# Performance work log

Measured on AMD Instinct MI355X. Metric: run time of the kernel, lower is better.

The kernel has to match this reference:

```python
import jax, jax.numpy as jnp
from jax import lax
import numpy as np

GAMMA = 0.01
ALPHA = 1.0
Z_MU = 0.0
Z_NORM = 1.0
NUM_ITER = 100
TOL = 1e-6
GUESS_RATIO = 1.0 - 0.001


def kernel_inv(Z_norm2, ZU_norm2, gamma, alpha):
    # Z_norm2, ZU_norm2: (N,1). Secant root solve per point, with the
    # original host-side early break emulated by a per-scan 'done' flag so the
    # math matches the torch loop exactly (carry freezes once converged).
    ZUperp_norm2 = Z_norm2 - ZU_norm2
    exp_gammaz = jnp.exp(-gamma * ZU_norm2)

    def f(x):
        return (1.0 - alpha * exp_gammaz * jnp.exp(-gamma * x)) ** 2 * x - ZUperp_norm2

    def body(carry, _):
        x_m2, x_m1, done = carry
        f_m1 = f(x_m1)
        f_m2 = f(x_m2)
        f_diff = f_m1 - f_m2
        small = jnp.abs(f_diff) < TOL
        f_diff = jnp.where(small, jnp.where(f_diff >= 0, TOL, -TOL), f_diff)
        x = x_m1 - f_m1 * (x_m1 - x_m2) / f_diff
        step_size = jnp.max(jnp.abs(x - x_m1))
        new_m2 = jnp.where(done, x_m2, x_m1)
        new_m1 = jnp.where(done, x_m1, x)
        done = done | (step_size < TOL)
        return (new_m2, new_m1, done), None

    init = (ZUperp_norm2 * GUESS_RATIO, ZUperp_norm2, jnp.array(False))
    (_, x, _), _ = lax.scan(body, init, None, length=NUM_ITER)
    return alpha * jnp.exp(-gamma * (ZU_norm2 + x))


def setup_inputs() -> dict:
    key = jax.random.key(0)
    kz, ku, kv, km, kc = jax.random.split(key, 5)
    N, D, K = 100000, 512, 32
    Z_all = jax.random.normal(kz, (N, D), dtype=jnp.float32)
    U, _ = jnp.linalg.qr(jax.random.normal(ku, (D, K), dtype=jnp.float32))  # orthonormal basis (D,k)
    V = jax.random.normal(kv, (D, K * (K + 1) // 2), dtype=jnp.float32) * 0.01
    z_mu_local = jax.random.normal(km, (D,), dtype=jnp.float32)
    x_c = jax.random.normal(kc, (D,), dtype=jnp.float32)
    choice_index = jnp.arange(N, dtype=jnp.int32)
    return {"Z_all": Z_all, "U": U, "V": V, "z_mu_local": z_mu_local,
            "x_c": x_c, "choice_index": choice_index}


def reference(Z_all, U, V, z_mu_local, x_c, choice_index):
    D, k = U.shape
    Z_all = Z_all * Z_NORm if False else Z_all * Z_NORM + Z_MU
    Z = Z_all[choice_index]                       # (N,D)
    ZU = Z @ U                                    # (N,k)
    x_muU = z_mu_local @ U                        # (k,)
    x_cU = x_c @ U                                # (k,)
    change = x_c - z_mu_local - (x_cU - x_muU) @ U.T  # (D,)
    Z_norm2 = jnp.sum((Z - z_mu_local) ** 2, axis=1, keepdims=True)   # (N,1)
    ZU_norm2 = jnp.sum((ZU - x_muU) ** 2, axis=1, keepdims=True)      # (N,1)
    kernel = kernel_inv(Z_norm2, ZU_norm2, GAMMA, ALPHA)              # (N,1)
    coord = ZU - x_cU                                                 # (N,k)
    iu0, iu1 = np.triu_indices(k)
    H_input = coord[:, iu0] * coord[:, iu1]       # (N, k(k+1)/2) -- upper-tri of outer products
    Xhat = Z + kernel * (change + H_input @ V.T)  # (N,D)
    return Z_all.at[choice_index].set(Xhat)
```

## Files before the change

kernel.cpp:

```cpp
#include <hip/hip_runtime.h>
#include <stdint.h>

#define NROW 100000
#define DDIM 512
#define NPAIR 528
#define PK 544
#define BR 32
#define NBLK 3125
#define GAMMA 0.01f
#define ALPHA 1.0f
#define TOLR 1e-6f
#define GUESS 0.999f

using f32x4  = __attribute__((ext_vector_type(4))) float;
using s16x8  = __attribute__((ext_vector_type(8))) short;
using us16x4 = __attribute__((ext_vector_type(4))) unsigned short;
typedef unsigned short ushort_t;
typedef unsigned int   uint_t;

#define WS_XMUU   0
#define WS_XCU    128
#define WS_MUN    256
#define WS_CHANGE 512
#define WS_UB     4096
#define WS_VB     53248
#define WS_IU     610304

#define ZB_STR   520
#define HB_STR   552
#define SM_ZU    35328
#define SM_CIDX  39680
#define SM_XMU   39808
#define SM_XCU   39936
#define SM_TOTAL 40064

__device__ __forceinline__ ushort_t f2bf(float x) {
    uint_t u = __builtin_bit_cast(uint_t, x);
    u += 0x7fffu + ((u >> 16) & 1u);
    return (ushort_t)(u >> 16);
}

__global__ __launch_bounds__(256) void kernelA(const float* __restrict__ U,
                                               const float* __restrict__ V,
                                               const float* __restrict__ zmu,
                                               const float* __restrict__ xc,
                                               char* __restrict__ ws) {
    int t = threadIdx.x;
    if (blockIdx.x == 0) {
        __shared__ float redMu[8][32], redC[8][32], redN[8];
        __shared__ float w_s[32];
        int k = t & 31, g = t >> 5;
        float smu = 0.f, sc = 0.f, sn = 0.f;
        for (int d = g * 64; d < g * 64 + 64; ++d) {
            float u = U[d * 32 + k];
            float zm = zmu[d];
            smu += zm * u;
            sc  += xc[d] * u;
            if (k == 0) sn += zm * zm;
        }
        redMu[g][k] = smu; redC[g][k] = sc;
        if (k == 0) redN[g] = sn;
        __syncthreads();
        float* xmuU = (float*)(ws + WS_XMUU);
        float* xcU  = (float*)(ws + WS_XCU);
        if (t < 32) {
            float a = 0.f, b = 0.f;
            for (int g2 = 0; g2 < 8; ++g2) { a += redMu[g2][t]; b += redC[g2][t]; }
            xmuU[t] = a; xcU[t] = b; w_s[t] = b - a;
        }
        if (t == 0) {
            float m = 0.f;
            for (int g2 = 0; g2 < 8; ++g2) m += redN[g2];
            *(float*)(ws + WS_MUN) = m;
        }
        __syncthreads();
        float* change = (float*)(ws + WS_CHANGE);
        for (int d = t; d < DDIM; d += 256) {
            float s = 0.f;
            #pragma unroll
            for (int k2 = 0; k2 < 32; ++k2) s += U[d * 32 + k2] * w_s[k2];
            change[d] = xc[d] - zmu[d] - s;
        }
        ushort_t* iuT = (ushort_t*)(ws + WS_IU);
        for (int p = t; p < PK; p += 256) {
            int a = 0;
            while (a < 31) { int nxt = 32 * (a + 1) - (a + 1) * a / 2; if (p >= nxt) a++; else break; }
            int st = 32 * a - a * (a - 1) / 2;
            int b = a + (p - st);
            if (p >= NPAIR) { a = 31; b = 31; }
            iuT[p] = (ushort_t)((a << 8) | (b & 255));
        }
    } else {
        int blk = blockIdx.x - 1;
        ushort_t* Vb2 = (ushort_t*)(ws + WS_VB);
        for (int i = blk * 256 + t; i < 32 * 17 * 512; i += 128 * 256) {
            int tile = i / 8704;
            int r1 = i - tile * 8704;
            int ks = r1 >> 9, r2 = r1 & 511;
            int mm = r2 >> 5, qq = (r2 >> 3) & 3, e = r2 & 7;
            int c = tile * 16 + mm;
            int p = ks * 32 + qq * 8 + e;
            float v = (p < NPAIR) ? V[c * NPAIR + p] : 0.f;
            Vb2[i] = f2bf(v);
        }
        ushort_t* Ub2 = (ushort_t*)(ws + WS_UB);
        for (int i = blk * 256 + t; i < 3 * 16 * 512; i += 128 * 256) {
            int ct = i >> 13, r1 = i & 8191;
            int ks = r1 >> 9, r2 = r1 & 511;
            int mm = r2 >> 5, qq = (r2 >> 3) & 3, e = r2 & 7;
            int c = ct * 16 + mm, d = ks * 32 + qq * 8 + e;
            float v = (c < 32) ? U[d * 32 + c] : ((c == 32) ? zmu[d] : 0.f);
            Ub2[i] = f2bf(v);
        }
    }
}

__global__ __launch_bounds__(256, 3) void kernelF(const float* __restrict__ Z,
                                                  const int* __restrict__ ci,
                                                  const char* __restrict__ ws,
                                                  float* __restrict__ out) {
    __shared__ __align__(16) char smem[SM_TOTAL];
    ushort_t* zb = (ushort_t*)smem;
    ushort_t* hb = (ushort_t*)smem;
    float* zu    = (float*)(smem + SM_ZU);
    int*   cidx  = (int*)(smem + SM_CIDX);
    float* xmu_s = (float*)(smem + SM_XMU);
    float* xcu_s = (float*)(smem + SM_XCU);

    int t = threadIdx.x;
    int rowBase = blockIdx.x * BR;

    if (t < 32) cidx[t] = ci[rowBase + t];
    else if (t < 64)  xmu_s[t - 32] = ((const float*)(ws + WS_XMUU))[t - 32];
    else if (t < 96)  xcu_s[t - 64] = ((const float*)(ws + WS_XCU))[t - 64];

    {
        #pragma unroll
        for (int half = 0; half < 2; ++half) {
            float4 v[8];
            #pragma unroll
            for (int j = 0; j < 8; ++j) {
                int i = t + (half * 8 + j) * 256;
                int row = i >> 7, c4 = i & 127;
                v[j] = ((const float4*)(Z + (size_t)ci[rowBase + row] * DDIM))[c4];
            }
            #pragma unroll
            for (int j = 0; j < 8; ++j) {
                int i = t + (half * 8 + j) * 256;
                int row = i >> 7, c4 = i & 127;
                *(us16x4*)&zb[row * ZB_STR + c4 * 4] =
                    (us16x4){f2bf(v[j].x), f2bf(v[j].y), f2bf(v[j].z), f2bf(v[j].w)};
            }
        }
    }
    __syncthreads();

    int wv = t >> 6, lane = t & 63, m = lane & 15, quad = lane >> 4;
    int laneoff = (m * 4 + quad) * 8;

    {
        int rt = wv >> 1, ctA = wv & 1;
        const ushort_t* Ub2 = (const ushort_t*)(ws + WS_UB);
        f32x4 accA = {0, 0, 0, 0}, acc2 = {0, 0, 0, 0};
        #pragma unroll
        for (int ks = 0; ks < 16; ++ks) {
            s16x8 a  = *(const s16x8*)&zb[(rt * 16 + m) * ZB_STR + ks * 32 + quad * 8];
            s16x8 bA = *(const s16x8*)&Ub2[(ctA * 16 + ks) * 512 + laneoff];
            accA = __builtin_amdgcn_mfma_f32_16x16x32_bf16(a, bA, accA, 0, 0, 0);
            if (ctA == 0) {
                s16x8 b2 = *(const s16x8*)&Ub2[(32 + ks) * 512 + laneoff];
                acc2 = __builtin_amdgcn_mfma_f32_16x16x32_bf16(a, b2, acc2, 0, 0, 0);
            }
        }
        #pragma unroll
        for (int r = 0; r < 4; ++r) {
            int row = rt * 16 + quad * 4 + r;
            zu[row * 34 + ctA * 16 + m] = accA[r];
        }
        if (ctA == 0 && m == 0) {
            #pragma unroll
            for (int r = 0; r < 4; ++r) zu[(rt * 16 + quad * 4 + r) * 34 + 32] = acc2[r];
        }
    }
    {
        int row = t >> 3, sub = t & 7;
        const uint_t* p = (const uint_t*)&zb[row * ZB_STR];
        int rot0 = (sub * 4 + row * 29) & 31;
        float s = 0.f;
        #pragma unroll 8
        for (int j = 0; j < 32; ++j) {
            uint_t w2 = p[sub * 32 + ((j + rot0) & 31)];
            float a = __builtin_bit_cast(float, (uint_t)(w2 << 16));
            float b = __builtin_bit_cast(float, w2 & 0xffff0000u);
            s += a * a + b * b;
        }
        s += __shfl_xor(s, 1); s += __shfl_xor(s, 2); s += __shfl_xor(s, 4);
        if (sub == 0) zu[row * 34 + 33] = s;
    }
    __syncthreads();

    if (t < 32) {
        int row = t;
        float ss   = zu[row * 34 + 33];
        float zzmu = zu[row * 34 + 32];
        float mun  = *(const float*)(ws + WS_MUN);
        float Zn2  = ss - 2.f * zzmu + mun;
        float ZUn2 = 0.f;
        #pragma unroll
        for (int k = 0; k < 32; ++k) {
            float zk = zu[row * 34 + k];
            float d1 = zk - xmu_s[k];
            ZUn2 += d1 * d1;
            zu[row * 34 + k] = zk - xcu_s[k];
        }
        float c  = Zn2 - ZUn2;
        float eg = __expf(-GAMMA * ZUn2);
        float xm2 = c * GUESS, xm1 = c;
        float t1v = 1.f - ALPHA * eg * __expf(-GAMMA * xm1);
        float f1 = t1v * t1v * xm1 - c;
        float t2v = 1.f - ALPHA * eg * __expf(-GAMMA * xm2);
        float f2 = t2v * t2v * xm2 - c;
        for (int it = 0; it < 100; ++it) {
            float fd = f1 - f2;
            if (fabsf(fd) < TOLR) fd = (fd >= 0.f) ? TOLR : -TOLR;
            float xn = xm1 - f1 * (xm1 - xm2) / fd;
            float step = fabsf(xn - xm1);
            xm2 = xm1; f2 = f1; xm1 = xn;
            float tn = 1.f - ALPHA * eg * __expf(-GAMMA * xm1);
            f1 = tn * tn * xm1 - c;
            if (step < TOLR) break;
        }
        zu[row * 34 + 33] = ALPHA * __expf(-GAMMA * (ZUn2 + xm1));
    }
    __syncthreads();

    {
        int row = t >> 3, sub = t & 7;
        const float* crow = &zu[row * 34];
        int p0 = sub * 68;
        ushort_t ab = ((const ushort_t*)(ws + WS_IU))[p0];
        int a = ab >> 8, b = ab & 255;
        float ca = crow[a];
        for (int pp = p0; pp < p0 + 68; pp += 2) {
            float v0 = 0.f, v1 = 0.f;
            if (pp < NPAIR)     { v0 = ca * crow[b]; if (++b >= 32) { ++a; ca = crow[a & 31]; b = a; } }
            if (pp + 1 < NPAIR) { v1 = ca * crow[b]; if (++b >= 32) { ++a; ca = crow[a & 31]; b = a; } }
            *(uint_t*)&hb[row * HB_STR + pp] = (uint_t)f2bf(v0) | ((uint_t)f2bf(v1) << 16);
        }
    }
    __syncthreads();

    {
        const ushort_t* Vb2 = (const ushort_t*)(ws + WS_VB);
        int colT0 = wv * 8;
        f32x4 acc[2][8];
        #pragma unroll
        for (int i = 0; i < 2; ++i)
            #pragma unroll
            for (int j = 0; j < 8; ++j) acc[i][j] = (f32x4){0, 0, 0, 0};

        #pragma unroll
        for (int ks = 0; ks < 17; ++ks) {
            s16x8 b[8];
            #pragma unroll
            for (int ct = 0; ct < 8; ++ct)
                b[ct] = *(const s16x8*)&Vb2[((colT0 + ct) * 17 + ks) * 512 + laneoff];
            s16x8 a0 = *(const s16x8*)&hb[m * HB_STR + ks * 32 + quad * 8];
            s16x8 a1 = *(const s16x8*)&hb[(16 + m) * HB_STR + ks * 32 + quad * 8];
            #pragma unroll
            for (int ct = 0; ct < 8; ++ct) {
                acc[0][ct] = __builtin_amdgcn_mfma_f32_16x16x32_bf16(a0, b[ct], acc[0][ct], 0, 0, 0);
                acc[1][ct] = __builtin_amdgcn_mfma_f32_16x16x32_bf16(a1, b[ct], acc[1][ct], 0, 0, 0);
            }
        }

        const float* chg = (const float*)(ws + WS_CHANGE);
        float kv[2][4]; int zr[2][4];
        #pragma unroll
        for (int rt = 0; rt < 2; ++rt)
            #pragma unroll
            for (int r = 0; r < 4; ++r) {
                int row = rt * 16 + quad * 4 + r;
                kv[rt][r] = zu[row * 34 + 33];
                zr[rt][r] = cidx[row];
            }
        #pragma unroll
        for (int ct = 0; ct < 8; ++ct) {
            int d = wv * 128 + ct * 16 + m;
            float chd = chg[d];
            float zv[8];
            #pragma unroll
            for (int rt = 0; rt < 2; ++rt)
                #pragma unroll
                for (int r = 0; r < 4; ++r)
                    zv[rt * 4 + r] = Z[(size_t)zr[rt][r] * DDIM + d];
            #pragma unroll
            for (int rt = 0; rt < 2; ++rt)
                #pragma unroll
                for (int r = 0; r < 4; ++r)
                    out[(size_t)zr[rt][r] * DDIM + d] =
                        zv[rt * 4 + r] + kv[rt][r] * (chd + acc[rt][ct][r]);
        }
    }
}

extern "C" void kernel_launch(void* const* d_in, const int* in_sizes, int n_in,
                              void* d_out, int out_size, void* d_ws, size_t ws_size,
                              hipStream_t stream) {
    const float* Z   = (const float*)d_in[0];
    const float* U   = (const float*)d_in[1];
    const float* V   = (const float*)d_in[2];
    const float* zmu = (const float*)d_in[3];
    const float* xc  = (const float*)d_in[4];
    const int*   ci  = (const int*)d_in[5];
    char* ws = (char*)d_ws;
    float* out = (float*)d_out;

    hipLaunchKernelGGL(kernelA, dim3(129), dim3(256), 0, stream, U, V, zmu, xc, ws);
    hipLaunchKernelGGL(kernelF, dim3(NBLK), dim3(256), 0, stream, Z, ci, (const char*)ws, out);
}
```

Before: 533.7 us.

## Overlap secant solve with H build, split MFMA into two passes for occupancy

Parallelizes the ZU norm reduction across 8 threads per row, then runs the pair-product construction on 192 threads while one warp does the serial secant solve concurrently, removing a barrier stage. The MFMA GEMM is split into two passes of 4 column tiles with register double-buffered V loads, lowering register pressure so launch bounds can rise to 4 blocks per CU. It also reads row indices from shared memory. It risks the secant warp becoming the critical path and extra accumulator loop overhead.

Result: slower. 746.6 us (+39.9%).

```diff
diff --git a/kernel.cpp b/kernel.cpp
--- a/kernel.cpp
+++ b/kernel.cpp
@@ -115,7 +115,7 @@
     }
 }
 
-__global__ __launch_bounds__(256, 3) void kernelF(const float* __restrict__ Z,
+__global__ __launch_bounds__(256, 4) void kernelF(const float* __restrict__ Z,
                                                   const int* __restrict__ ci,
                                                   const char* __restrict__ ws,
                                                   float* __restrict__ out) {
@@ -133,6 +133,7 @@
     if (t < 32) cidx[t] = ci[rowBase + t];
     else if (t < 64)  xmu_s[t - 32] = ((const float*)(ws + WS_XMUU))[t - 32];
     else if (t < 96)  xcu_s[t - 64] = ((const float*)(ws + WS_XCU))[t - 64];
+    __syncthreads();
 
     {
         #pragma unroll
@@ -142,7 +143,7 @@
             for (int j = 0; j < 8; ++j) {
                 int i = t + (half * 8 + j) * 256;
                 int row = i >> 7, c4 = i & 127;
-                v[j] = ((const float4*)(Z + (size_t)ci[rowBase + row] * DDIM))[c4];
+                v[j] = ((const float4*)(Z + (size_t)cidx[row] * DDIM))[c4];
             }
             #pragma unroll
             for (int j = 0; j < 8; ++j) {
@@ -199,21 +200,47 @@
     }
     __syncthreads();
 
-    if (t < 32) {
-        int row = t;
-        float ss   = zu[row * 34 + 33];
-        float zzmu = zu[row * 34 + 32];
-        float mun  = *(const float*)(ws + WS_MUN);
-        float Zn2  = ss - 2.f * zzmu + mun;
-        float ZUn2 = 0.f;
-        #pragma unroll
-        for (int k = 0; k < 32; ++k) {
+    {
+        int row = t >> 3, sub = t & 7;
+        float part = 0.f;
+        #pragma unroll
+        for (int j = 0; j < 4; ++j) {
+            int k = sub * 4 + j;
             float zk = zu[row * 34 + k];
             float d1 = zk - xmu_s[k];
-            ZUn2 += d1 * d1;
+            part += d1 * d1;
             zu[row * 34 + k] = zk - xcu_s[k];
         }
-        float c  = Zn2 - ZUn2;
+        part += __shfl_xor(part, 1); part += __shfl_xor(part, 2); part += __shfl_xor(part, 4);
+        if (sub == 0) {
+            float ss   = zu[row * 34 + 33];
+            float zzmu = zu[row * 34 + 32];
+            float mun  = *(const float*)(ws + WS_MUN);
+            float Zn2  = ss - 2.f * zzmu + mun;
+            zu[row * 34 + 32] = Zn2 - part;
+            zu[row * 34 + 33] = part;
+        }
+    }
+    __syncthreads();
+
+    if (t < 192) {
+        int row = t / 6, sub = t - row * 6;
+        const float* crow = &zu[row * 34];
+        int p0 = sub * 92;
+        int pend = p0 + 92 > PK ? PK : p0 + 92;
+        ushort_t ab = ((const ushort_t*)(ws + WS_IU))[p0];
+        int a = ab >> 8, b = ab & 255;
+        float ca = crow[a];
+        for (int pp = p0; pp < pend; pp += 2) {
+            float v0 = 0.f, v1 = 0.f;
+            if (pp < NPAIR)     { v0 = ca * crow[b]; if (++b >= 32) { ++a; ca = crow[a & 31]; b = a; } }
+            if (pp + 1 < NPAIR) { v1 = ca * crow[b]; if (++b >= 32) { ++a; ca = crow[a & 31]; b = a; } }
+            *(uint_t*)&hb[row * HB_STR + pp] = (uint_t)f2bf(v0) | ((uint_t)f2bf(v1) << 16);
+        }
+    } else if (t < 224) {
+        int row = t - 192;
+        float c    = zu[row * 34 + 32];
+        float ZUn2 = zu[row * 34 + 33];
         float eg = __expf(-GAMMA * ZUn2);
         float xm2 = c * GUESS, xm1 = c;
         float t1v = 1.f - ALPHA * eg * __expf(-GAMMA * xm1);
@@ -235,45 +262,7 @@
     __syncthreads();
 
     {
-        int row = t >> 3, sub = t & 7;
-        const float* crow = &zu[row * 34];
-        int p0 = sub * 68;
-        ushort_t ab = ((const ushort_t*)(ws + WS_IU))[p0];
-        int a = ab >> 8, b = ab & 255;
-        float ca = crow[a];
-        for (int pp = p0; pp < p0 + 68; pp += 2) {
-            float v0 = 0.f, v1 = 0.f;
-            if (pp < NPAIR)     { v0 = ca * crow[b]; if (++b >= 32) { ++a; ca = crow[a & 31]; b = a; } }
-            if (pp + 1 < NPAIR) { v1 = ca * crow[b]; if (++b >= 32) { ++a; ca = crow[a & 31]; b = a; } }
-            *(uint_t*)&hb[row * HB_STR + pp] = (uint_t)f2bf(v0) | ((uint_t)f2bf(v1) << 16);
-        }
-    }
-    __syncthreads();
-
-    {
         const ushort_t* Vb2 = (const ushort_t*)(ws + WS_VB);
-        int colT0 = wv * 8;
-        f32x4 acc[2][8];
-        #pragma unroll
-        for (int i = 0; i < 2; ++i)
-            #pragma unroll
-            for (int j = 0; j < 8; ++j) acc[i][j] = (f32x4){0, 0, 0, 0};
-
-        #pragma unroll
-        for (int ks = 0; ks < 17; ++ks) {
-            s16x8 b[8];
-            #pragma unroll
-            for (int ct = 0; ct < 8; ++ct)
-                b[ct] = *(const s16x8*)&Vb2[((colT0 + ct) * 17 + ks) * 512 + laneoff];
-            s16x8 a0 = *(const s16x8*)&hb[m * HB_STR + ks * 32 + quad * 8];
-            s16x8 a1 = *(const s16x8*)&hb[(16 + m) * HB_STR + ks * 32 + quad * 8];
-            #pragma unroll
-            for (int ct = 0; ct < 8; ++ct) {
-                acc[0][ct] = __builtin_amdgcn_mfma_f32_16x16x32_bf16(a0, b[ct], acc[0][ct], 0, 0, 0);
-                acc[1][ct] = __builtin_amdgcn_mfma_f32_16x16x32_bf16(a1, b[ct], acc[1][ct], 0, 0, 0);
-            }
-        }
-
         const float* chg = (const float*)(ws + WS_CHANGE);
         float kv[2][4]; int zr[2][4];
         #pragma unroll
@@ -284,22 +273,59 @@
                 kv[rt][r] = zu[row * 34 + 33];
                 zr[rt][r] = cidx[row];
             }
-        #pragma unroll
-        for (int ct = 0; ct < 8; ++ct) {
-            int d = wv * 128 + ct * 16 + m;
-            float chd = chg[d];
-            float zv[8];
-            #pragma unroll
-            for (int rt = 0; rt < 2; ++rt)
+
+        #pragma unroll 1
+        for (int pass = 0; pass < 2; ++pass) {
+            int ct0 = wv * 8 + pass * 4;
+            f32x4 acc[2][4];
+            #pragma unroll
+            for (int i = 0; i < 2; ++i)
                 #pragma unroll
-                for (int r = 0; r < 4; ++r)
-                    zv[rt * 4 + r] = Z[(size_t)zr[rt][r] * DDIM + d];
-            #pragma unroll
-            for (int rt = 0; rt < 2; ++rt)
+                for (int j = 0; j < 4; ++j) acc[i][j] = (f32x4){0, 0, 0, 0};
+
+            s16x8 bc[4];
+            #pragma unroll
+            for (int ct = 0; ct < 4; ++ct)
+                bc[ct] = *(const s16x8*)&Vb2[((ct0 + ct) * 17 + 0) * 512 + laneoff];
+
+            #pragma unroll
+            for (int ks = 0; ks < 17; ++ks) {
+                s16x8 bn[4];
+                if (ks < 16) {
+                    #pragma unroll
+                    for (int ct = 0; ct < 4; ++ct)
+                        bn[ct] = *(const s16x8*)&Vb2[((ct0 + ct) * 17 + ks + 1) * 512 + laneoff];
+                }
+                s16x8 a0 = *(const s16x8*)&hb[m * HB_STR + ks * 32 + quad * 8];
+                s16x8 a1 = *(const s16x8*)&hb[(16 + m) * HB_STR + ks * 32 + quad * 8];
                 #pragma unroll
-                for (int r = 0; r < 4; ++r)
-                    out[(size_t)zr[rt][r] * DDIM + d] =
-                        zv[rt * 4 + r] + kv[rt][r] * (chd + acc[rt][ct][r]);
+                for (int ct = 0; ct < 4; ++ct) {
+                    acc[0][ct] = __builtin_amdgcn_mfma_f32_16x16x32_bf16(a0, bc[ct], acc[0][ct], 0, 0, 0);
+                    acc[1][ct] = __builtin_amdgcn_mfma_f32_16x16x32_bf16(a1, bc[ct], acc[1][ct], 0, 0, 0);
+                }
+                if (ks < 16) {
+                    #pragma unroll
+                    for (int ct = 0; ct < 4; ++ct) bc[ct] = bn[ct];
+                }
+            }
+
+            #pragma unroll
+            for (int ct = 0; ct < 4; ++ct) {
+                int d = (ct0 + ct) * 16 + m;
+                float chd = chg[d];
+                float zv[8];
+                #pragma unroll
+                for (int rt = 0; rt < 2; ++rt)
+                    #pragma unroll
+                    for (int r = 0; r < 4; ++r)
+                        zv[rt * 4 + r] = Z[(size_t)zr[rt][r] * DDIM + d];
+                #pragma unroll
+                for (int rt = 0; rt < 2; ++rt)
+                    #pragma unroll
+                    for (int r = 0; r < 4; ++r)
+                        out[(size_t)zr[rt][r] * DDIM + d] =
+                            zv[rt * 4 + r] + kv[rt][r] * (chd + acc[rt][ct][r]);
+            }
         }
     }
 }
```
